# Kernel optimization log

Measured on AMD Instinct MI355X. Metric: run time of the kernel, lower is better.

The kernel has to match this reference:

```python
import jax, jax.numpy as jnp
import numpy as np
import math

B, L, D, ALPHA = 8, 4096, 1024, 64
EPS = 1e-6

def _xavier(key, shape):
    fan_in, fan_out = shape[1], shape[0]
    bound = math.sqrt(6.0 / (fan_in + fan_out))
    return jax.random.uniform(key, shape, jnp.float32, -bound, bound)

def layer_norm(x, g, b):
    # matches the torch module: unbiased std, divide by (std + eps)
    mean = jnp.mean(x, axis=-1, keepdims=True)
    var = jnp.sum((x - mean) ** 2, axis=-1, keepdims=True) / (x.shape[-1] - 1)
    std = jnp.sqrt(var)
    return g * (x - mean) / (std + EPS) + b

def setup_inputs() -> dict:
    key = jax.random.key(0)
    ks = jax.random.split(key, 8)
    x = jax.random.normal(ks[0], (B, L, D), jnp.float32)
    mask = jnp.ones((B, L), jnp.int32)
    W_Q = _xavier(ks[1], (D, D))          # torch Linear weight [out, in]
    b_Q = jnp.zeros((D,), jnp.float32)
    C_K = _xavier(ks[2], (D, ALPHA))
    C_V = _xavier(ks[3], (D, ALPHA))
    g1 = jnp.ones((D,), jnp.float32)
    be1 = jnp.zeros((D,), jnp.float32)
    Wc = _xavier(ks[4], (D, D))           # 1x1 conv weight squeezed: [out, in]
    bc = jax.random.normal(ks[5], (D,), jnp.float32) * 0.02
    g2 = jnp.ones((D,), jnp.float32)
    be2 = jnp.zeros((D,), jnp.float32)
    return {"x": x, "mask": mask, "W_Q": W_Q, "b_Q": b_Q, "C_K": C_K,
            "C_V": C_V, "g1": g1, "be1": be1, "Wc": Wc, "bc": bc,
            "g2": g2, "be2": be2}

def reference(x, mask, W_Q, b_Q, C_K, C_V, g1, be1, Wc, bc, g2, be2):
    d = x.shape[-1]
    # CoLAttention: Q = Linear(x); A = softmax(Q @ C_K / sqrt(D)); out = A @ C_V^T
    Q = jnp.einsum('bld,ed->ble', x, W_Q) + b_Q
    A = jax.nn.softmax(jnp.einsum('bld,da->bla', Q, C_K) / math.sqrt(d), axis=-1)
    A = A * mask[:, :, None].astype(A.dtype)
    attn = jnp.einsum('bla,da->bld', A, C_V)   # (dropout = 0)
    # Add & Norm
    h = layer_norm(x + attn, g1, be1)
    # PointWise 1x1 conv FFN: conv -> LeakyReLU -> (dropout=0) -> Add & Norm
    conv = jnp.einsum('bld,ed->ble', h, Wc) + bc
    act = jax.nn.leaky_relu(conv, negative_slope=0.01)
    out = layer_norm(h + act, g2, be2)
    return out
```

## Files before the change

kernel.cpp:

```cpp
#include <hip/hip_runtime.h>
#include <stdint.h>


#define NTHREADS 512

typedef float  f32x4  __attribute__((ext_vector_type(4)));
typedef short  s16x8  __attribute__((ext_vector_type(8)));
typedef __bf16 bf16x8 __attribute__((ext_vector_type(8)));

__device__ __forceinline__ uint16_t f2bf(float f) {
  uint32_t b = __builtin_bit_cast(uint32_t, f);
  b += 0x7FFFu + ((b >> 16) & 1u);
  return (uint16_t)(b >> 16);
}
__device__ __forceinline__ float bf2f(uint16_t u) {
  return __builtin_bit_cast(float, ((uint32_t)u) << 16);
}
__device__ __forceinline__ f32x4 MFMA(s16x8 a, s16x8 b, f32x4 c) {
  return __builtin_amdgcn_mfma_f32_16x16x32_bf16(
      __builtin_bit_cast(bf16x8, a), __builtin_bit_cast(bf16x8, b), c, 0, 0, 0);
}

__global__ void k0_m(const float* __restrict__ WQ, const float* __restrict__ CK,
                     uint16_t* __restrict__ MbfT) {
  __shared__ float wq[32][16];
  __shared__ float ck[32][64];
  const int t  = threadIdx.x;
  const int d0 = blockIdx.x * 16;
  const int a  = t >> 2, dq = t & 3;
  float acc[4] = {0.f, 0.f, 0.f, 0.f};
  for (int e0 = 0; e0 < 1024; e0 += 32) {
    {
      int i0 = t * 2, r = i0 >> 4, c = i0 & 15;
      float2 v = *(const float2*)(WQ + (size_t)(e0 + r) * 1024 + d0 + c);
      wq[r][c] = v.x; wq[r][c + 1] = v.y;
    }
#pragma unroll
    for (int j = 0; j < 8; j++) {
      int idx = t + j * 256, r = idx >> 6, c = idx & 63;
      ck[r][c] = CK[(size_t)(e0 + r) * 64 + c];
    }
    __syncthreads();
    for (int r = 0; r < 32; r++) {
      float cv = ck[r][a];
#pragma unroll
      for (int i = 0; i < 4; i++) acc[i] += cv * wq[r][dq * 4 + i];
    }
    __syncthreads();
  }
#pragma unroll
  for (int i = 0; i < 4; i++) {
    int d = d0 + dq * 4 + i;
    MbfT[(size_t)a * 1024 + d] = f2bf(acc[i] * 0.03125f);
  }
}

__global__ void k0_s0(const float* __restrict__ bQ, const float* __restrict__ CK,
                      float* __restrict__ s0) {
  __shared__ float part[4][64];
  const int t = threadIdx.x, a = t & 63, q = t >> 6;
  float s = 0.f;
  for (int e = q * 256; e < (q + 1) * 256; e++) s += bQ[e] * CK[(size_t)e * 64 + a];
  part[q][a] = s;
  __syncthreads();
  if (q == 0) s0[a] = (part[0][a] + part[1][a] + part[2][a] + part[3][a]) * 0.03125f;
}

__global__ void k0_cvt(const float* __restrict__ CV, const float* __restrict__ Wc,
                       uint16_t* __restrict__ CVbf, uint16_t* __restrict__ Wcbf) {
  int i4 = blockIdx.x * 256 + threadIdx.x;
  const float4* src;
  uint16_t* dst;
  if (i4 < 16384) { src = (const float4*)CV; dst = CVbf; }
  else            { src = (const float4*)Wc; dst = Wcbf; i4 -= 16384; }
  float4 v = src[i4];
  uint32_t lo = (uint32_t)f2bf(v.x) | ((uint32_t)f2bf(v.y) << 16);
  uint32_t hi = (uint32_t)f2bf(v.z) | ((uint32_t)f2bf(v.w) << 16);
  uint2 pk; pk.x = lo; pk.y = hi;
  *(uint2*)(dst + (size_t)i4 * 4) = pk;
}

__global__ __launch_bounds__(NTHREADS, 2) void fused_main(
    const float* __restrict__ x, const int* __restrict__ mask,
    const float* __restrict__ s0, const uint16_t* __restrict__ MbfT,
    const uint16_t* __restrict__ CVbf, const uint16_t* __restrict__ Wcbf,
    const float* __restrict__ g1, const float* __restrict__ be1,
    const float* __restrict__ bc, const float* __restrict__ g2,
    const float* __restrict__ be2, float* __restrict__ out) {
  extern __shared__ char smem[];
  char*  xs    = smem;
  char*  asmb  = smem + 131072;
  float* Ssm   = (float*)(smem + 139264);
  float* stats = (float*)(smem + 131072);

  const int tid = threadIdx.x;
  const int w = tid >> 6, l = tid & 63;
  const int ln = l & 15, kg = l >> 4;
  const size_t tok0 = (size_t)blockIdx.x * 64;

  {
    const float* xg = x + tok0 * 1024;
#pragma unroll
    for (int i = 0; i < 16; i++) {
      int g = tid + i * NTHREADS;
      int row = g >> 7, c8 = g & 127;
      const float4* p = (const float4*)(xg + (size_t)row * 1024 + c8 * 8);
      float vb[8];
      *(float4*)(vb) = p[0]; *(float4*)(vb + 4) = p[1];
      s16x8 pk;
#pragma unroll
      for (int e = 0; e < 8; e++) pk[e] = (short)f2bf(vb[e]);
      uint32_t ad = (uint32_t)(row * 2048 + c8 * 16) ^ ((uint32_t)(row & 7) << 4);
      *(s16x8*)(xs + ad) = pk;
    }
  }
  __syncthreads();

  {
    const int rt = w >> 1;
    const int c0 = ((w & 1) * 2) * 16 + ln;
    const int c1 = ((w & 1) * 2 + 1) * 16 + ln;
    f32x4 sa0 = {0.f, 0.f, 0.f, 0.f}, sa1 = {0.f, 0.f, 0.f, 0.f};
    for (int ks = 0; ks < 32; ks++) {
      int row = rt * 16 + ln;
      uint32_t ad = (uint32_t)(row * 2048 + ks * 64 + kg * 16) ^ ((uint32_t)(row & 7) << 4);
      s16x8 af = *(const s16x8*)(xs + ad);
      s16x8 b0 = *(const s16x8*)(MbfT + (size_t)c0 * 1024 + ks * 32 + kg * 8);
      s16x8 b1 = *(const s16x8*)(MbfT + (size_t)c1 * 1024 + ks * 32 + kg * 8);
      sa0 = MFMA(af, b0, sa0);
      sa1 = MFMA(af, b1, sa1);
    }
#pragma unroll
    for (int r = 0; r < 4; r++) {
      int row = rt * 16 + kg * 4 + r;
      Ssm[row * 64 + c0] = sa0[r] + s0[c0];
      Ssm[row * 64 + c1] = sa1[r] + s0[c1];
    }
  }
  __syncthreads();

  {
    int row = tid >> 3, g8 = tid & 7;
    float v[8];
#pragma unroll
    for (int i = 0; i < 8; i++) v[i] = Ssm[row * 64 + g8 * 8 + i];
    float m = v[0];
#pragma unroll
    for (int i = 1; i < 8; i++) m = fmaxf(m, v[i]);
    m = fmaxf(m, __shfl_xor(m, 1));
    m = fmaxf(m, __shfl_xor(m, 2));
    m = fmaxf(m, __shfl_xor(m, 4));
    float s = 0.f;
#pragma unroll
    for (int i = 0; i < 8; i++) { v[i] = __expf(v[i] - m); s += v[i]; }
    s += __shfl_xor(s, 1); s += __shfl_xor(s, 2); s += __shfl_xor(s, 4);
    float inv = (float)mask[tok0 + row] / s;
    s16x8 pk;
#pragma unroll
    for (int i = 0; i < 8; i++) pk[i] = (short)f2bf(v[i] * inv);
    uint32_t ad = (uint32_t)(row * 128 + g8 * 16) ^ ((uint32_t)(row & 7) << 4);
    *(s16x8*)(asmb + ad) = pk;
  }
  __syncthreads();

  {
    f32x4 acc[4][8];
#pragma unroll
    for (int a_ = 0; a_ < 4; a_++)
#pragma unroll
      for (int b_ = 0; b_ < 8; b_++) acc[a_][b_] = f32x4{0.f, 0.f, 0.f, 0.f};
#pragma unroll
    for (int ks = 0; ks < 2; ks++) {
      s16x8 af[4];
#pragma unroll
      for (int rt = 0; rt < 4; rt++) {
        int row = rt * 16 + ln;
        uint32_t ad = (uint32_t)(row * 128 + ks * 64 + kg * 16) ^ ((uint32_t)(row & 7) << 4);
        af[rt] = *(const s16x8*)(asmb + ad);
      }
#pragma unroll
      for (int cc = 0; cc < 8; cc++) {
        int dcol = (w * 8 + cc) * 16 + ln;
        s16x8 bf = *(const s16x8*)(CVbf + (size_t)dcol * 64 + ks * 32 + kg * 8);
#pragma unroll
        for (int rt = 0; rt < 4; rt++) acc[rt][cc] = MFMA(af[rt], bf, acc[rt][cc]);
      }
    }
#pragma unroll
    for (int cc = 0; cc < 8; cc++) {
      int col = (w * 8 + cc) * 16 + ln;
#pragma unroll
      for (int rt = 0; rt < 4; rt++)
#pragma unroll
        for (int r = 0; r < 4; r++) {
          int row = rt * 16 + kg * 4 + r;
          uint32_t ad = (uint32_t)(row * 2048 + col * 2) ^ ((uint32_t)(row & 7) << 4);
          float xv = bf2f(*(const uint16_t*)(xs + ad));
          *(uint16_t*)(xs + ad) = f2bf(xv + acc[rt][cc][r]);
        }
    }
  }
  __syncthreads();

  {
    int row = tid >> 3, g8 = tid & 7;
    float sum = 0.f, sq = 0.f;
#pragma unroll
    for (int i = 0; i < 16; i++) {
      uint32_t ad = (uint32_t)(row * 2048 + (g8 * 16 + i) * 16) ^ ((uint32_t)(row & 7) << 4);
      s16x8 vv = *(const s16x8*)(xs + ad);
#pragma unroll
      for (int e = 0; e < 8; e++) { float f = bf2f((uint16_t)vv[e]); sum += f; sq += f * f; }
    }
    sum += __shfl_xor(sum, 1); sum += __shfl_xor(sum, 2); sum += __shfl_xor(sum, 4);
    sq  += __shfl_xor(sq, 1);  sq  += __shfl_xor(sq, 2);  sq  += __shfl_xor(sq, 4);
    float mean = sum * (1.0f / 1024.0f);
    float var  = fmaxf((sq - 1024.0f * mean * mean) * (1.0f / 1023.0f), 0.f);
    float rinv = 1.0f / (sqrtf(var) + 1e-6f);
#pragma unroll
    for (int i = 0; i < 16; i++) {
      uint32_t ad = (uint32_t)(row * 2048 + (g8 * 16 + i) * 16) ^ ((uint32_t)(row & 7) << 4);
      s16x8 vv = *(const s16x8*)(xs + ad);
      int col0 = g8 * 128 + i * 8;
      s16x8 hv;
#pragma unroll
      for (int e = 0; e < 8; e++) {
        float f = bf2f((uint16_t)vv[e]);
        hv[e] = (short)f2bf(g1[col0 + e] * (f - mean) * rinv + be1[col0 + e]);
      }
      *(s16x8*)(xs + ad) = hv;
    }
  }
  __syncthreads();

  {
    f32x4 acc[4][8];
#pragma unroll
    for (int a_ = 0; a_ < 4; a_++)
#pragma unroll
      for (int b_ = 0; b_ < 8; b_++) acc[a_][b_] = f32x4{0.f, 0.f, 0.f, 0.f};
    for (int ks = 0; ks < 32; ks++) {
      s16x8 af[4];
#pragma unroll
      for (int rt = 0; rt < 4; rt++) {
        int row = rt * 16 + ln;
        uint32_t ad = (uint32_t)(row * 2048 + ks * 64 + kg * 16) ^ ((uint32_t)(row & 7) << 4);
        af[rt] = *(const s16x8*)(xs + ad);
      }
#pragma unroll
      for (int cc = 0; cc < 8; cc++) {
        int ecol = (w * 8 + cc) * 16 + ln;
        s16x8 bf = *(const s16x8*)(Wcbf + (size_t)ecol * 1024 + ks * 32 + kg * 8);
#pragma unroll
        for (int rt = 0; rt < 4; rt++) acc[rt][cc] = MFMA(af[rt], bf, acc[rt][cc]);
      }
    }
    __syncthreads();
#pragma unroll
    for (int cc = 0; cc < 8; cc++) {
      int col = (w * 8 + cc) * 16 + ln;
      float bcv = bc[col];
#pragma unroll
      for (int rt = 0; rt < 4; rt++)
#pragma unroll
        for (int r = 0; r < 4; r++) {
          int row = rt * 16 + kg * 4 + r;
          float conv = acc[rt][cc][r] + bcv;
          float act  = conv > 0.f ? conv : 0.01f * conv;
          uint32_t ad = (uint32_t)(row * 2048 + col * 2) ^ ((uint32_t)(row & 7) << 4);
          float h = bf2f(*(const uint16_t*)(xs + ad));
          *(uint16_t*)(xs + ad) = f2bf(h + act);
        }
    }
  }
  __syncthreads();

  {
    int row = tid >> 3, g8 = tid & 7;
    float sum = 0.f, sq = 0.f;
#pragma unroll
    for (int i = 0; i < 16; i++) {
      uint32_t ad = (uint32_t)(row * 2048 + (g8 * 16 + i) * 16) ^ ((uint32_t)(row & 7) << 4);
      s16x8 vv = *(const s16x8*)(xs + ad);
#pragma unroll
      for (int e = 0; e < 8; e++) { float f = bf2f((uint16_t)vv[e]); sum += f; sq += f * f; }
    }
    sum += __shfl_xor(sum, 1); sum += __shfl_xor(sum, 2); sum += __shfl_xor(sum, 4);
    sq  += __shfl_xor(sq, 1);  sq  += __shfl_xor(sq, 2);  sq  += __shfl_xor(sq, 4);
    float mean = sum * (1.0f / 1024.0f);
    float var  = fmaxf((sq - 1024.0f * mean * mean) * (1.0f / 1023.0f), 0.f);
    float rinv = 1.0f / (sqrtf(var) + 1e-6f);
    if (g8 == 0) { stats[row * 2] = mean; stats[row * 2 + 1] = rinv; }
  }
  __syncthreads();

  {
#pragma unroll
    for (int i = 0; i < 16; i++) {
      int g = tid + i * NTHREADS;
      int row = g >> 7, c8 = g & 127;
      uint32_t ad = (uint32_t)(row * 2048 + c8 * 16) ^ ((uint32_t)(row & 7) << 4);
      s16x8 vv = *(const s16x8*)(xs + ad);
      float mean = stats[row * 2], rinv = stats[row * 2 + 1];
      int col0 = c8 * 8;
      float ov[8];
#pragma unroll
      for (int e = 0; e < 8; e++) {
        float f = bf2f((uint16_t)vv[e]);
        ov[e] = g2[col0 + e] * (f - mean) * rinv + be2[col0 + e];
      }
      float* op = out + (tok0 + row) * 1024 + col0;
      *(float4*)op = *(float4*)(ov);
      *(float4*)(op + 4) = *(float4*)(ov + 4);
    }
  }
}

extern "C" void kernel_launch(void* const* d_in, const int* in_sizes, int n_in,
                              void* d_out, int out_size, void* d_ws, size_t ws_size,
                              hipStream_t stream) {
  const float* x   = (const float*)d_in[0];
  const int*   msk = (const int*)d_in[1];
  const float* WQ  = (const float*)d_in[2];
  const float* bQ  = (const float*)d_in[3];
  const float* CK  = (const float*)d_in[4];
  const float* CV  = (const float*)d_in[5];
  const float* g1  = (const float*)d_in[6];
  const float* be1 = (const float*)d_in[7];
  const float* Wc  = (const float*)d_in[8];
  const float* bc  = (const float*)d_in[9];
  const float* g2  = (const float*)d_in[10];
  const float* be2 = (const float*)d_in[11];
  float* out = (float*)d_out;

  char* ws = (char*)d_ws;
  uint16_t* Wcbf = (uint16_t*)ws;
  uint16_t* MbfT = (uint16_t*)(ws + 2097152);
  uint16_t* CVbf = (uint16_t*)(ws + 2228224);
  float*    s0   = (float*)(ws + 2359296);

  (void)hipFuncSetAttribute((const void*)fused_main,
                            hipFuncAttributeMaxDynamicSharedMemorySize, 155648);

  k0_m  <<<64,   256, 0, stream>>>(WQ, CK, MbfT);
  k0_s0 <<<1,    256, 0, stream>>>(bQ, CK, s0);
  k0_cvt<<<1088, 256, 0, stream>>>(CV, Wc, CVbf, Wcbf);
  fused_main<<<512, NTHREADS, 155648, stream>>>(x, msk, s0, MbfT, CVbf, Wcbf,
                                                g1, be1, bc, g2, be2, out);
}
```

Baseline: 513.4 us.

## Fold LayerNorm1 into conv weights, double block size, fuse softmax and prep kernels

```diff
diff --git a/kernel.cpp b/kernel.cpp
--- a/kernel.cpp
+++ b/kernel.cpp
@@ -2,10 +2,11 @@
 #include <stdint.h>
 
 
-#define NTHREADS 512
+#define NT 1024
 
 typedef float  f32x4  __attribute__((ext_vector_type(4)));
 typedef short  s16x8  __attribute__((ext_vector_type(8)));
+typedef short  s16x4  __attribute__((ext_vector_type(4)));
 typedef __bf16 bf16x8 __attribute__((ext_vector_type(8)));
 
 __device__ __forceinline__ uint16_t f2bf(float f) {
@@ -21,297 +22,317 @@
       __builtin_bit_cast(bf16x8, a), __builtin_bit_cast(bf16x8, b), c, 0, 0, 0);
 }
 
-__global__ void k0_m(const float* __restrict__ WQ, const float* __restrict__ CK,
-                     uint16_t* __restrict__ MbfT) {
-  __shared__ float wq[32][16];
-  __shared__ float ck[32][64];
-  const int t  = threadIdx.x;
-  const int d0 = blockIdx.x * 16;
-  const int a  = t >> 2, dq = t & 3;
-  float acc[4] = {0.f, 0.f, 0.f, 0.f};
-  for (int e0 = 0; e0 < 1024; e0 += 32) {
-    {
-      int i0 = t * 2, r = i0 >> 4, c = i0 & 15;
-      float2 v = *(const float2*)(WQ + (size_t)(e0 + r) * 1024 + d0 + c);
-      wq[r][c] = v.x; wq[r][c + 1] = v.y;
-    }
-#pragma unroll
-    for (int j = 0; j < 8; j++) {
-      int idx = t + j * 256, r = idx >> 6, c = idx & 63;
-      ck[r][c] = CK[(size_t)(e0 + r) * 64 + c];
-    }
+__global__ void k0_all(const float* __restrict__ WQ, const float* __restrict__ bQ,
+                       const float* __restrict__ CK, const float* __restrict__ CV,
+                       const float* __restrict__ Wc, const float* __restrict__ g1,
+                       const float* __restrict__ be1, const float* __restrict__ bc,
+                       uint16_t* __restrict__ MbfT, float* __restrict__ s0,
+                       uint16_t* __restrict__ CVbf, uint16_t* __restrict__ Wpbf,
+                       float* __restrict__ u, float* __restrict__ vb) {
+  __shared__ float sm[2560];
+  const int b = blockIdx.x, t = threadIdx.x;
+  if (b < 64) {
+    float (*wq)[16] = (float(*)[16])sm;
+    float (*ck)[64] = (float(*)[64])(sm + 512);
+    const int d0 = b * 16, a = t >> 2, dq = t & 3;
+    float acc[4] = {0.f, 0.f, 0.f, 0.f};
+    for (int e0 = 0; e0 < 1024; e0 += 32) {
+      {
+        int i0 = t * 2, r = i0 >> 4, c = i0 & 15;
+        float2 v = *(const float2*)(WQ + (size_t)(e0 + r) * 1024 + d0 + c);
+        wq[r][c] = v.x; wq[r][c + 1] = v.y;
+      }
+#pragma unroll
+      for (int j = 0; j < 8; j++) {
+        int idx = t + j * 256, r = idx >> 6, c = idx & 63;
+        ck[r][c] = CK[(size_t)(e0 + r) * 64 + c];
+      }
+      __syncthreads();
+      for (int r = 0; r < 32; r++) {
+        float cv = ck[r][a];
+#pragma unroll
+        for (int i = 0; i < 4; i++) acc[i] += cv * wq[r][dq * 4 + i];
+      }
+      __syncthreads();
+    }
+#pragma unroll
+    for (int i = 0; i < 4; i++)
+      MbfT[(size_t)a * 1024 + d0 + dq * 4 + i] = f2bf(acc[i] * 0.03125f);
+  } else if (b < 1152) {
+    int i4 = (b - 64) * 256 + t;
+    if (i4 < 16384) {
+      float4 v = ((const float4*)CV)[i4];
+      uint2 pk;
+      pk.x = (uint32_t)f2bf(v.x) | ((uint32_t)f2bf(v.y) << 16);
+      pk.y = (uint32_t)f2bf(v.z) | ((uint32_t)f2bf(v.w) << 16);
+      *(uint2*)(CVbf + (size_t)i4 * 4) = pk;
+    } else {
+      int f4 = i4 - 16384;
+      int d = (f4 * 4) & 1023;
+      float4 v = ((const float4*)Wc)[f4];
+      float4 g = *(const float4*)(g1 + d);
+      v.x *= g.x; v.y *= g.y; v.z *= g.z; v.w *= g.w;
+      uint2 pk;
+      pk.x = (uint32_t)f2bf(v.x) | ((uint32_t)f2bf(v.y) << 16);
+      pk.y = (uint32_t)f2bf(v.z) | ((uint32_t)f2bf(v.w) << 16);
+      *(uint2*)(Wpbf + (size_t)f4 * 4) = pk;
+    }
+  } else if (b == 1152) {
+    float (*part)[64] = (float(*)[64])sm;
+    const int a = t & 63, q = t >> 6;
+    float s = 0.f;
+    for (int e = q * 256; e < (q + 1) * 256; e++) s += bQ[e] * CK[(size_t)e * 64 + a];
+    part[q][a] = s;
     __syncthreads();
-    for (int r = 0; r < 32; r++) {
-      float cv = ck[r][a];
-#pragma unroll
-      for (int i = 0; i < 4; i++) acc[i] += cv * wq[r][dq * 4 + i];
-    }
-    __syncthreads();
-  }
-#pragma unroll
-  for (int i = 0; i < 4; i++) {
-    int d = d0 + dq * 4 + i;
-    MbfT[(size_t)a * 1024 + d] = f2bf(acc[i] * 0.03125f);
-  }
-}
-
-__global__ void k0_s0(const float* __restrict__ bQ, const float* __restrict__ CK,
-                      float* __restrict__ s0) {
-  __shared__ float part[4][64];
-  const int t = threadIdx.x, a = t & 63, q = t >> 6;
-  float s = 0.f;
-  for (int e = q * 256; e < (q + 1) * 256; e++) s += bQ[e] * CK[(size_t)e * 64 + a];
-  part[q][a] = s;
-  __syncthreads();
-  if (q == 0) s0[a] = (part[0][a] + part[1][a] + part[2][a] + part[3][a]) * 0.03125f;
-}
-
-__global__ void k0_cvt(const float* __restrict__ CV, const float* __restrict__ Wc,
-                       uint16_t* __restrict__ CVbf, uint16_t* __restrict__ Wcbf) {
-  int i4 = blockIdx.x * 256 + threadIdx.x;
-  const float4* src;
-  uint16_t* dst;
-  if (i4 < 16384) { src = (const float4*)CV; dst = CVbf; }
-  else            { src = (const float4*)Wc; dst = Wcbf; i4 -= 16384; }
-  float4 v = src[i4];
-  uint32_t lo = (uint32_t)f2bf(v.x) | ((uint32_t)f2bf(v.y) << 16);
-  uint32_t hi = (uint32_t)f2bf(v.z) | ((uint32_t)f2bf(v.w) << 16);
-  uint2 pk; pk.x = lo; pk.y = hi;
-  *(uint2*)(dst + (size_t)i4 * 4) = pk;
-}
-
-__global__ __launch_bounds__(NTHREADS, 2) void fused_main(
+    if (q == 0) s0[a] = (part[0][a] + part[1][a] + part[2][a] + part[3][a]) * 0.03125f;
+  } else {
+    const int e = (b - 1153) * 4 + (t >> 6), l = t & 63;
+    float su = 0.f, sv = 0.f;
+#pragma unroll
+    for (int j = 0; j < 16; j++) {
+      int d = l + 64 * j;
+      float w = Wc[(size_t)e * 1024 + d];
+      su += g1[d] * w;
+      sv += be1[d] * w;
+    }
+#pragma unroll
+    for (int m = 1; m <= 32; m <<= 1) { su += __shfl_xor(su, m); sv += __shfl_xor(sv, m); }
+    if (l == 0) { u[e] = su; vb[e] = sv + bc[e]; }
+  }
+}
+
+__global__ __launch_bounds__(NT, 4) void fused_main(
     const float* __restrict__ x, const int* __restrict__ mask,
     const float* __restrict__ s0, const uint16_t* __restrict__ MbfT,
-    const uint16_t* __restrict__ CVbf, const uint16_t* __restrict__ Wcbf,
+    const uint16_t* __restrict__ CVbf, const uint16_t* __restrict__ Wpbf,
+    const float* __restrict__ u, const float* __restrict__ vb,
     const float* __restrict__ g1, const float* __restrict__ be1,
-    const float* __restrict__ bc, const float* __restrict__ g2,
-    const float* __restrict__ be2, float* __restrict__ out) {
+    const float* __restrict__ g2, const float* __restrict__ be2,
+    float* __restrict__ out) {
   extern __shared__ char smem[];
-  char*  xs    = smem;
-  char*  asmb  = smem + 131072;
-  float* Ssm   = (float*)(smem + 139264);
-  float* stats = (float*)(smem + 131072);
+  char*   xs    = smem;
+  char*   asmb  = smem + 131072;
+  float2* part  = (float2*)(smem + 139264);
+  float*  stats = (float*)(smem + 147456);
 
   const int tid = threadIdx.x;
   const int w = tid >> 6, l = tid & 63;
   const int ln = l & 15, kg = l >> 4;
   const size_t tok0 = (size_t)blockIdx.x * 64;
+  const int E0 = w * 64;
 
   {
     const float* xg = x + tok0 * 1024;
 #pragma unroll
-    for (int i = 0; i < 16; i++) {
-      int g = tid + i * NTHREADS;
+    for (int i = 0; i < 8; i++) {
+      int g = tid + i * NT;
       int row = g >> 7, c8 = g & 127;
       const float4* p = (const float4*)(xg + (size_t)row * 1024 + c8 * 8);
-      float vb[8];
-      *(float4*)(vb) = p[0]; *(float4*)(vb + 4) = p[1];
+      float vbuf[8];
+      *(float4*)(vbuf) = p[0]; *(float4*)(vbuf + 4) = p[1];
       s16x8 pk;
 #pragma unroll
-      for (int e = 0; e < 8; e++) pk[e] = (short)f2bf(vb[e]);
+      for (int e = 0; e < 8; e++) pk[e] = (short)f2bf(vbuf[e]);
       uint32_t ad = (uint32_t)(row * 2048 + c8 * 16) ^ ((uint32_t)(row & 7) << 4);
       *(s16x8*)(xs + ad) = pk;
     }
   }
   __syncthreads();
 
+  if (w < 4) {
+    const int tokr = w * 16 + ln;
+    f32x4 accs[4];
+#pragma unroll
+    for (int at = 0; at < 4; at++) accs[at] = f32x4{0.f, 0.f, 0.f, 0.f};
+    for (int ks = 0; ks < 32; ks++) {
+      uint32_t ad = (uint32_t)(tokr * 2048 + ks * 64 + kg * 16) ^ ((uint32_t)(tokr & 7) << 4);
+      s16x8 bfr = *(const s16x8*)(xs + ad);
+#pragma unroll
+      for (int at = 0; at < 4; at++) {
+        s16x8 af = *(const s16x8*)(MbfT + (size_t)(at * 16 + ln) * 1024 + ks * 32 + kg * 8);
+        accs[at] = MFMA(af, bfr, accs[at]);
+      }
+    }
+    float v[4][4], mx = -1e30f;
+#pragma unroll
+    for (int at = 0; at < 4; at++) {
+      float4 s4 = *(const float4*)(s0 + at * 16 + kg * 4);
+      const float* sp = (const float*)&s4;
+#pragma unroll
+      for (int r = 0; r < 4; r++) { v[at][r] = accs[at][r] + sp[r]; mx = fmaxf(mx, v[at][r]); }
+    }
+    mx = fmaxf(mx, __shfl_xor(mx, 16));
+    mx = fmaxf(mx, __shfl_xor(mx, 32));
+    float s = 0.f;
+#pragma unroll
+    for (int at = 0; at < 4; at++)
+#pragma unroll
+      for (int r = 0; r < 4; r++) { v[at][r] = __expf(v[at][r] - mx); s += v[at][r]; }
+    s += __shfl_xor(s, 16);
+    s += __shfl_xor(s, 32);
+    float inv = (float)mask[tok0 + tokr] / s;
+#pragma unroll
+    for (int at = 0; at < 4; at++) {
+      s16x4 pk;
+#pragma unroll
+      for (int r = 0; r < 4; r++) pk[r] = (short)f2bf(v[at][r] * inv);
+      uint32_t ad = (uint32_t)(tokr * 128 + at * 32 + kg * 8) ^ ((uint32_t)(tokr & 7) << 4);
+      *(s16x4*)(asmb + ad) = pk;
+    }
+  }
+  __syncthreads();
+
+  float st[4], sq[4];
   {
-    const int rt = w >> 1;
-    const int c0 = ((w & 1) * 2) * 16 + ln;
-    const int c1 = ((w & 1) * 2 + 1) * 16 + ln;
-    f32x4 sa0 = {0.f, 0.f, 0.f, 0.f}, sa1 = {0.f, 0.f, 0.f, 0.f};
+    f32x4 acc[4][4];
+#pragma unroll
+    for (int et = 0; et < 4; et++)
+#pragma unroll
+      for (int tt = 0; tt < 4; tt++) acc[et][tt] = f32x4{0.f, 0.f, 0.f, 0.f};
+#pragma unroll
+    for (int ks = 0; ks < 2; ks++) {
+      s16x8 bfr[4];
+#pragma unroll
+      for (int tt = 0; tt < 4; tt++) {
+        int tokr = tt * 16 + ln;
+        uint32_t ad = (uint32_t)(tokr * 128 + ks * 64 + kg * 16) ^ ((uint32_t)(tokr & 7) << 4);
+        bfr[tt] = *(const s16x8*)(asmb + ad);
+      }
+#pragma unroll
+      for (int et = 0; et < 4; et++) {
+        s16x8 af = *(const s16x8*)(CVbf + (size_t)(E0 + et * 16 + ln) * 64 + ks * 32 + kg * 8);
+#pragma unroll
+        for (int tt = 0; tt < 4; tt++) acc[et][tt] = MFMA(af, bfr[tt], acc[et][tt]);
+      }
+    }
+#pragma unroll
+    for (int tt = 0; tt < 4; tt++) { st[tt] = 0.f; sq[tt] = 0.f; }
+#pragma unroll
+    for (int et = 0; et < 4; et++)
+#pragma unroll
+      for (int tt = 0; tt < 4; tt++) {
+        int tokr = tt * 16 + ln;
+        int d = E0 + et * 16 + kg * 4;
+        uint32_t ad = (uint32_t)(tokr * 2048 + d * 2) ^ ((uint32_t)(tokr & 7) << 4);
+        s16x4 xv = *(const s16x4*)(xs + ad);
+        s16x4 hv;
+#pragma unroll
+        for (int r = 0; r < 4; r++) {
+          float h = bf2f((uint16_t)xv[r]) + acc[et][tt][r];
+          st[tt] += h; sq[tt] += h * h;
+          hv[r] = (short)f2bf(h);
+        }
+        *(s16x4*)(xs + ad) = hv;
+      }
+#pragma unroll
+    for (int tt = 0; tt < 4; tt++) {
+      st[tt] += __shfl_xor(st[tt], 16); st[tt] += __shfl_xor(st[tt], 32);
+      sq[tt] += __shfl_xor(sq[tt], 16); sq[tt] += __shfl_xor(sq[tt], 32);
+    }
+    if (kg == 0) {
+#pragma unroll
+      for (int tt = 0; tt < 4; tt++) part[w * 64 + tt * 16 + ln] = float2{st[tt], sq[tt]};
+    }
+  }
+  __syncthreads();
+  if (tid < 64) {
+    float s = 0.f, q = 0.f;
+#pragma unroll
+    for (int ww = 0; ww < 16; ww++) { float2 p = part[ww * 64 + tid]; s += p.x; q += p.y; }
+    float mean = s * (1.0f / 1024.0f);
+    float var  = fmaxf((q - 1024.0f * mean * mean) * (1.0f / 1023.0f), 0.f);
+    stats[tid * 2] = mean;
+    stats[tid * 2 + 1] = 1.0f / (sqrtf(var) + 1e-6f);
+  }
+  __syncthreads();
+
+  {
+    f32x4 acc[4][4];
+#pragma unroll
+    for (int et = 0; et < 4; et++)
+#pragma unroll
+      for (int tt = 0; tt < 4; tt++) acc[et][tt] = f32x4{0.f, 0.f, 0.f, 0.f};
     for (int ks = 0; ks < 32; ks++) {
-      int row = rt * 16 + ln;
-      uint32_t ad = (uint32_t)(row * 2048 + ks * 64 + kg * 16) ^ ((uint32_t)(row & 7) << 4);
-      s16x8 af = *(const s16x8*)(xs + ad);
-      s16x8 b0 = *(const s16x8*)(MbfT + (size_t)c0 * 1024 + ks * 32 + kg * 8);
-      s16x8 b1 = *(const s16x8*)(MbfT + (size_t)c1 * 1024 + ks * 32 + kg * 8);
-      sa0 = MFMA(af, b0, sa0);
-      sa1 = MFMA(af, b1, sa1);
-    }
-#pragma unroll
-    for (int r = 0; r < 4; r++) {
-      int row = rt * 16 + kg * 4 + r;
-      Ssm[row * 64 + c0] = sa0[r] + s0[c0];
-      Ssm[row * 64 + c1] = sa1[r] + s0[c1];
-    }
-  }
-  __syncthreads();
-
-  {
-    int row = tid >> 3, g8 = tid & 7;
-    float v[8];
-#pragma unroll
-    for (int i = 0; i < 8; i++) v[i] = Ssm[row * 64 + g8 * 8 + i];
-    float m = v[0];
-#pragma unroll
-    for (int i = 1; i < 8; i++) m = fmaxf(m, v[i]);
-    m = fmaxf(m, __shfl_xor(m, 1));
-    m = fmaxf(m, __shfl_xor(m, 2));
-    m = fmaxf(m, __shfl_xor(m, 4));
-    float s = 0.f;
-#pragma unroll
-    for (int i = 0; i < 8; i++) { v[i] = __expf(v[i] - m); s += v[i]; }
-    s += __shfl_xor(s, 1); s += __shfl_xor(s, 2); s += __shfl_xor(s, 4);
-    float inv = (float)mask[tok0 + row] / s;
-    s16x8 pk;
-#pragma unroll
-    for (int i = 0; i < 8; i++) pk[i] = (short)f2bf(v[i] * inv);
-    uint32_t ad = (uint32_t)(row * 128 + g8 * 16) ^ ((uint32_t)(row & 7) << 4);
-    *(s16x8*)(asmb + ad) = pk;
-  }
-  __syncthreads();
-
-  {
-    f32x4 acc[4][8];
-#pragma unroll
-    for (int a_ = 0; a_ < 4; a_++)
-#pragma unroll
-      for (int b_ = 0; b_ < 8; b_++) acc[a_][b_] = f32x4{0.f, 0.f, 0.f, 0.f};
-#pragma unroll
-    for (int ks = 0; ks < 2; ks++) {
-      s16x8 af[4];
-#pragma unroll
-      for (int rt = 0; rt < 4; rt++) {
-        int row = rt * 16 + ln;
-        uint32_t ad = (uint32_t)(row * 128 + ks * 64 + kg * 16) ^ ((uint32_t)(row & 7) << 4);
-        af[rt] = *(const s16x8*)(asmb + ad);
-      }
-#pragma unroll
-      for (int cc = 0; cc < 8; cc++) {
-        int dcol = (w * 8 + cc) * 16 + ln;
-        s16x8 bf = *(const s16x8*)(CVbf + (size_t)dcol * 64 + ks * 32 + kg * 8);
-#pragma unroll
-        for (int rt = 0; rt < 4; rt++) acc[rt][cc] = MFMA(af[rt], bf, acc[rt][cc]);
-      }
-    }
-#pragma unroll
-    for (int cc = 0; cc < 8; cc++) {
-      int col = (w * 8 + cc) * 16 + ln;
-#pragma unroll
-      for (int rt = 0; rt < 4; rt++)
+      s16x8 bfr[4];
+#pragma unroll
+      for (int tt = 0; tt < 4; tt++) {
+        int tokr = tt * 16 + ln;
+        uint32_t ad = (uint32_t)(tokr * 2048 + ks * 64 + kg * 16) ^ ((uint32_t)(tokr & 7) << 4);
+        bfr[tt] = *(const s16x8*)(xs + ad);
+      }
+#pragma unroll
+      for (int et = 0; et < 4; et++) {
+        s16x8 af = *(const s16x8*)(Wpbf + (size_t)(E0 + et * 16 + ln) * 1024 + ks * 32 + kg * 8);
+#pragma unroll
+        for (int tt = 0; tt < 4; tt++) acc[et][tt] = MFMA(af, bfr[tt], acc[et][tt]);
+      }
+    }
+#pragma unroll
+    for (int tt = 0; tt < 4; tt++) { st[tt] = 0.f; sq[tt] = 0.f; }
+#pragma unroll
+    for (int et = 0; et < 4; et++) {
+      int e0 = E0 + et * 16 + kg * 4;
+      float4 u4 = *(const float4*)(u + e0);
+      float4 v4 = *(const float4*)(vb + e0);
+      float4 gg = *(const float4*)(g1 + e0);
+      float4 bb = *(const float4*)(be1 + e0);
+      const float *uf = (const float*)&u4, *vf = (const float*)&v4;
+      const float *gf = (const float*)&gg, *bf = (const float*)&bb;
+#pragma unroll
+      for (int tt = 0; tt < 4; tt++) {
+        int tokr = tt * 16 + ln;
+        float mean = stats[tokr * 2], rinv = stats[tokr * 2 + 1];
+        uint32_t ad = (uint32_t)(tokr * 2048 + e0 * 2) ^ ((uint32_t)(tokr & 7) << 4);
+        s16x4 hv = *(const s16x4*)(xs + ad);
 #pragma unroll
         for (int r = 0; r < 4; r++) {
-          int row = rt * 16 + kg * 4 + r;
-          uint32_t ad = (uint32_t)(row * 2048 + col * 2) ^ ((uint32_t)(row & 7) << 4);
-          float xv = bf2f(*(const uint16_t*)(xs + ad));
-          *(uint16_t*)(xs + ad) = f2bf(xv + acc[rt][cc][r]);
+          float conv = acc[et][tt][r] * rinv - rinv * mean * uf[r] + vf[r];
+          float act  = conv > 0.f ? conv : 0.01f * conv;
+          float h    = gf[r] * (bf2f((uint16_t)hv[r]) - mean) * rinv + bf[r];
+          float rr   = h + act;
+          acc[et][tt][r] = rr;
+          st[tt] += rr; sq[tt] += rr * rr;
         }
-    }
-  }
-  __syncthreads();
-
-  {
-    int row = tid >> 3, g8 = tid & 7;
-    float sum = 0.f, sq = 0.f;
-#pragma unroll
-    for (int i = 0; i < 16; i++) {
-      uint32_t ad = (uint32_t)(row * 2048 + (g8 * 16 + i) * 16) ^ ((uint32_t)(row & 7) << 4);
-      s16x8 vv = *(const s16x8*)(xs + ad);
-#pragma unroll
-      for (int e = 0; e < 8; e++) { float f = bf2f((uint16_t)vv[e]); sum += f; sq += f * f; }
-    }
-    sum += __shfl_xor(sum, 1); sum += __shfl_xor(sum, 2); sum += __shfl_xor(sum, 4);
-    sq  += __shfl_xor(sq, 1);  sq  += __shfl_xor(sq, 2);  sq  += __shfl_xor(sq, 4);
-    float mean = sum * (1.0f / 1024.0f);
-    float var  = fmaxf((sq - 1024.0f * mean * mean) * (1.0f / 1023.0f), 0.f);
-    float rinv = 1.0f / (sqrtf(var) + 1e-6f);
-#pragma unroll
-    for (int i = 0; i < 16; i++) {
-      uint32_t ad = (uint32_t)(row * 2048 + (g8 * 16 + i) * 16) ^ ((uint32_t)(row & 7) << 4);
-      s16x8 vv = *(const s16x8*)(xs + ad);
-      int col0 = g8 * 128 + i * 8;
-      s16x8 hv;
-#pragma unroll
-      for (int e = 0; e < 8; e++) {
-        float f = bf2f((uint16_t)vv[e]);
-        hv[e] = (short)f2bf(g1[col0 + e] * (f - mean) * rinv + be1[col0 + e]);
-      }
-      *(s16x8*)(xs + ad) = hv;
-    }
-  }
-  __syncthreads();
-
-  {
-    f32x4 acc[4][8];
-#pragma unroll
-    for (int a_ = 0; a_ < 4; a_++)
-#pragma unroll
-      for (int b_ = 0; b_ < 8; b_++) acc[a_][b_] = f32x4{0.f, 0.f, 0.f, 0.f};
-    for (int ks = 0; ks < 32; ks++) {
-      s16x8 af[4];
-#pragma unroll
-      for (int rt = 0; rt < 4; rt++) {
-        int row = rt * 16 + ln;
-        uint32_t ad = (uint32_t)(row * 2048 + ks * 64 + kg * 16) ^ ((uint32_t)(row & 7) << 4);
-        af[rt] = *(const s16x8*)(xs + ad);
-      }
-#pragma unroll
-      for (int cc = 0; cc < 8; cc++) {
-        int ecol = (w * 8 + cc) * 16 + ln;
-        s16x8 bf = *(const s16x8*)(Wcbf + (size_t)ecol * 1024 + ks * 32 + kg * 8);
-#pragma unroll
-        for (int rt = 0; rt < 4; rt++) acc[rt][cc] = MFMA(af[rt], bf, acc[rt][cc]);
-      }
+      }
+    }
+#pragma unroll
+    for (int tt = 0; tt < 4; tt++) {
+      st[tt] += __shfl_xor(st[tt], 16); st[tt] += __shfl_xor(st[tt], 32);
+      sq[tt] += __shfl_xor(sq[tt], 16); sq[tt] += __shfl_xor(sq[tt], 32);
+    }
+    if (kg == 0) {
+#pragma unroll
+      for (int tt = 0; tt < 4; tt++) part[w * 64 + tt * 16 + ln] = float2{st[tt], sq[tt]};
     }
     __syncthreads();
-#pragma unroll
-    for (int cc = 0; cc < 8; cc++) {
-      int col = (w * 8 + cc) * 16 + ln;
-      float bcv = bc[col];
-#pragma unroll
-      for (int rt = 0; rt < 4; rt++)
-#pragma unroll
-        for (int r = 0; r < 4; r++) {
-          int row = rt * 16 + kg * 4 + r;
-          float conv = acc[rt][cc][r] + bcv;
-          float act  = conv > 0.f ? conv : 0.01f * conv;
-          uint32_t ad = (uint32_t)(row * 2048 + col * 2) ^ ((uint32_t)(row & 7) << 4);
-          float h = bf2f(*(const uint16_t*)(xs + ad));
-          *(uint16_t*)(xs + ad) = f2bf(h + act);
-        }
-    }
-  }
-  __syncthreads();
-
-  {
-    int row = tid >> 3, g8 = tid & 7;
-    float sum = 0.f, sq = 0.f;
-#pragma unroll
-    for (int i = 0; i < 16; i++) {
-      uint32_t ad = (uint32_t)(row * 2048 + (g8 * 16 + i) * 16) ^ ((uint32_t)(row & 7) << 4);
-      s16x8 vv = *(const s16x8*)(xs + ad);
-#pragma unroll
-      for (int e = 0; e < 8; e++) { float f = bf2f((uint16_t)vv[e]); sum += f; sq += f * f; }
-    }
-    sum += __shfl_xor(sum, 1); sum += __shfl_xor(sum, 2); sum += __shfl_xor(sum, 4);
-    sq  += __shfl_xor(sq, 1);  sq  += __shfl_xor(sq, 2);  sq  += __shfl_xor(sq, 4);
-    float mean = sum * (1.0f / 1024.0f);
-    float var  = fmaxf((sq - 1024.0f * mean * mean) * (1.0f / 1023.0f), 0.f);
-    float rinv = 1.0f / (sqrtf(var) + 1e-6f);
-    if (g8 == 0) { stats[row * 2] = mean; stats[row * 2 + 1] = rinv; }
-  }
-  __syncthreads();
-
-  {
-#pragma unroll
-    for (int i = 0; i < 16; i++) {
-      int g = tid + i * NTHREADS;
-      int row = g >> 7, c8 = g & 127;
-      uint32_t ad = (uint32_t)(row * 2048 + c8 * 16) ^ ((uint32_t)(row & 7) << 4);
-      s16x8 vv = *(const s16x8*)(xs + ad);
-      float mean = stats[row * 2], rinv = stats[row * 2 + 1];
-      int col0 = c8 * 8;
-      float ov[8];
-#pragma unroll
-      for (int e = 0; e < 8; e++) {
-        float f = bf2f((uint16_t)vv[e]);
-        ov[e] = g2[col0 + e] * (f - mean) * rinv + be2[col0 + e];
-      }
-      float* op = out + (tok0 + row) * 1024 + col0;
-      *(float4*)op = *(float4*)(ov);
-      *(float4*)(op + 4) = *(float4*)(ov + 4);
+    if (tid < 64) {
+      float s = 0.f, q = 0.f;
+#pragma unroll
+      for (int ww = 0; ww < 16; ww++) { float2 p = part[ww * 64 + tid]; s += p.x; q += p.y; }
+      float mean = s * (1.0f / 1024.0f);
+      float var  = fmaxf((q - 1024.0f * mean * mean) * (1.0f / 1023.0f), 0.f);
+      stats[tid * 2] = mean;
+      stats[tid * 2 + 1] = 1.0f / (sqrtf(var) + 1e-6f);
+    }
+    __syncthreads();
+
+#pragma unroll
+    for (int et = 0; et < 4; et++) {
+      int e0 = E0 + et * 16 + kg * 4;
+      float4 gg = *(const float4*)(g2 + e0);
+      float4 bb = *(const float4*)(be2 + e0);
+      const float *gf = (const float*)&gg, *bf = (const float*)&bb;
+#pragma unroll
+      for (int tt = 0; tt < 4; tt++) {
+        int tokr = tt * 16 + ln;
+        float mean = stats[tokr * 2], rinv = stats[tokr * 2 + 1];
+        float4 o;
+        o.x = gf[0] * (acc[et][tt][0] - mean) * rinv + bf[0];
+        o.y = gf[1] * (acc[et][tt][1] - mean) * rinv + bf[1];
+        o.z = gf[2] * (acc[et][tt][2] - mean) * rinv + bf[2];
+        o.w = gf[3] * (acc[et][tt][3] - mean) * rinv + bf[3];
+        *(float4*)(out + (tok0 + tokr) * 1024 + e0) = o;
+      }
     }
   }
 }
@@ -334,17 +355,18 @@
   float* out = (float*)d_out;
 
   char* ws = (char*)d_ws;
-  uint16_t* Wcbf = (uint16_t*)ws;
+  uint16_t* Wpbf = (uint16_t*)ws;
   uint16_t* MbfT = (uint16_t*)(ws + 2097152);
   uint16_t* CVbf = (uint16_t*)(ws + 2228224);
   float*    s0   = (float*)(ws + 2359296);
+  float*    u    = (float*)(ws + 2359552);
+  float*    vb   = (float*)(ws + 2363648);
 
   (void)hipFuncSetAttribute((const void*)fused_main,
-                            hipFuncAttributeMaxDynamicSharedMemorySize, 155648);
-
-  k0_m  <<<64,   256, 0, stream>>>(WQ, CK, MbfT);
-  k0_s0 <<<1,    256, 0, stream>>>(bQ, CK, s0);
-  k0_cvt<<<1088, 256, 0, stream>>>(CV, Wc, CVbf, Wcbf);
-  fused_main<<<512, NTHREADS, 155648, stream>>>(x, msk, s0, MbfT, CVbf, Wcbf,
-                                                g1, be1, bc, g2, be2, out);
-}
+                            hipFuncAttributeMaxDynamicSharedMemorySize, 147968);
+
+  k0_all<<<1409, 256, 0, stream>>>(WQ, bQ, CK, CV, Wc, g1, be1, bc,
+                                   MbfT, s0, CVbf, Wpbf, u, vb);
+  fused_main<<<512, NT, 147968, stream>>>(x, msk, s0, MbfT, CVbf, Wpbf,
+                                          u, vb, g1, be1, g2, be2, out);
+}
```

After: 489.5 us. 4.7% less time.
